# Optimization experiments

Measured on AMD Instinct MI355X. Metric: run time of the kernel, lower is better.

## Reference

```python
import jax, jax.numpy as jnp
import numpy as np

N_NODES = 50000
N_EDGES = 800000
D_IN = 128
H = 4
F = 16


def setup_inputs() -> dict:
    key = jax.random.key(0)
    k1, k2, k3, k4 = jax.random.split(key, 4)
    feat = jax.random.normal(k1, (N_NODES, D_IN), dtype=jnp.float32)
    W = jax.random.normal(k2, (D_IN, H * F), dtype=jnp.float32) / np.sqrt(D_IN)
    src = jax.random.randint(k3, (N_EDGES,), 0, N_NODES, dtype=jnp.int32)
    dst = jax.random.randint(k4, (N_EDGES,), 0, N_NODES, dtype=jnp.int32)
    return {"feat": feat, "W": W, "src": src, "dst": dst}


def reference(feat, W, src, dst):
    # Project: [N, D_in] @ [D_in, H*F] -> [N, H, F]
    ft = (feat @ W).reshape(N_NODES, H, F)
    # Per-edge dot-product scores, scaled: [E, H]
    e = jnp.einsum('ehf,ehf->eh', ft[src], ft[dst]) / np.sqrt(F).astype(np.float32)
    # Segment (per-destination) softmax over incoming edges
    seg_max = jax.ops.segment_max(e, dst, num_segments=N_NODES)  # [N, H]
    ex = jnp.exp(e - seg_max[dst])
    denom = jax.ops.segment_sum(ex, dst, num_segments=N_NODES)  # [N, H]
    sa = ex / denom[dst]  # [E, H]
    # Weighted scatter-sum of source features: [N, H, F]
    msgs = ft[src] * sa[:, :, None]
    out = jax.ops.segment_sum(msgs, dst, num_segments=N_NODES)
    return out
```

## Files before the change

### kernel.cpp

```cpp
#include <hip/hip_runtime.h>
#include <hip/hip_fp16.h>

#define N_NODES 50000
#define N_EDGES 800000
#define D_IN 128
#define HH 4
#define FF 16
#define HF 64
#define NBUCKETS 392
#define BCAP 2560
#define CHUNK 2048
#define NBIN_BLOCKS ((N_EDGES + CHUNK - 1) / CHUNK)
#define GEMM_BLOCKS ((N_NODES + 63) / 64)
#define SORT_K (BCAP / 256)

struct __align__(8) Half4 { __half2 a, b; };

typedef _Float16 half2_v __attribute__((ext_vector_type(2)));
struct __align__(8) H4 { half2_v a, b; };

__device__ __forceinline__ float dot4h(H4 a, H4 v) {
#if __has_builtin(__builtin_amdgcn_fdot2)
    return __builtin_amdgcn_fdot2(a.a, v.a,
           __builtin_amdgcn_fdot2(a.b, v.b, 0.0f, false), false);
#else
    return (float)a.a[0] * (float)v.a[0] + (float)a.a[1] * (float)v.a[1]
         + (float)a.b[0] * (float)v.b[0] + (float)a.b[1] * (float)v.b[1];
#endif
}

__device__ __forceinline__ int block_excl_scan(int val, int* wsum) {
    int lane = threadIdx.x & 63;
    int wave = threadIdx.x >> 6;
    int incl = val;
#pragma unroll
    for (int off = 1; off < 64; off <<= 1) {
        int t = __shfl_up(incl, off, 64);
        if (lane >= off) incl += t;
    }
    if (lane == 63) wsum[wave] = incl;
    __syncthreads();
    if (threadIdx.x == 0) {
        int a = 0;
#pragma unroll
        for (int w = 0; w < 4; ++w) { int t = wsum[w]; wsum[w] = a; a += t; }
    }
    __syncthreads();
    return incl + wsum[wave] - val;
}

union SmemU {
    struct {
        float As[64][132];
        float Bs[D_IN][HF];
    } g;
    struct {
        int hist[512], cur[512], gbase[512];
    } b;
};

__global__ __launch_bounds__(256, 2) void gemm_bin_kernel(const float* __restrict__ feat,
                                                          const float* __restrict__ W,
                                                          const int* __restrict__ src,
                                                          const int* __restrict__ dst,
                                                          __half* __restrict__ fth,
                                                          int* __restrict__ gcur,
                                                          int* __restrict__ recs) {
    __shared__ SmemU smem;
    int tid = threadIdx.x;

    if (blockIdx.x < NBIN_BLOCKS) {
        int e0 = blockIdx.x * CHUNK;
        int n = N_EDGES - e0; if (n > CHUNK) n = CHUNK;

        smem.b.hist[tid] = 0;
        smem.b.hist[tid + 256] = 0;
        __syncthreads();

        int myrec[CHUNK / 256];
        int myb[CHUNK / 256];
#pragma unroll
        for (int k = 0; k < CHUNK / 256; ++k) {
            int idx = tid + k * 256;
            myb[k] = -1;
            if (idx < n) {
                int s = src[e0 + idx];
                int d = dst[e0 + idx];
                int b = d >> 7;
                myrec[k] = s | ((d & 127) << 16) | (b << 23);
                myb[k] = b;
                atomicAdd(&smem.b.hist[b], 1);
            }
        }
        __syncthreads();

#pragma unroll
        for (int j = 0; j < 2; ++j) {
            int idx = tid + j * 256;
            int val = smem.b.hist[idx];
            smem.b.cur[idx] = 0;
            if (val > 0) smem.b.gbase[idx] = atomicAdd(&gcur[idx], val);
        }
        __syncthreads();

#pragma unroll
        for (int k = 0; k < CHUNK / 256; ++k) {
            int b = myb[k];
            if (b >= 0) {
                int pos = smem.b.gbase[b] + atomicAdd(&smem.b.cur[b], 1);
                if (pos < BCAP) recs[(size_t)b * BCAP + pos] = myrec[k];
            }
        }
    } else {
        int gb = blockIdx.x - NBIN_BLOCKS;
        {
            const float4* W4 = (const float4*)W;
            float4* B4 = (float4*)smem.g.Bs;
#pragma unroll
            for (int i = 0; i < 8; ++i) {
                int idx = tid + 256 * i;
                B4[idx] = W4[idx];
            }
        }
        {
            int row0 = gb * 64;
            const float4* F4 = (const float4*)feat;
#pragma unroll
            for (int i = 0; i < 8; ++i) {
                int idx = tid + 256 * i;
                int r = idx >> 5;
                int c4 = idx & 31;
                float4 v = make_float4(0.f, 0.f, 0.f, 0.f);
                int row = row0 + r;
                if (row < N_NODES) v = F4[(size_t)row * 32 + c4];
                *(float4*)&smem.g.As[r][c4 * 4] = v;
            }
        }
        __syncthreads();

        const int tr = tid >> 4;
        const int tc = tid & 15;

        float acc[4][4] = {};
#pragma unroll 8
        for (int k = 0; k < D_IN; k += 4) {
            float av[4][4], bv[4][4];
#pragma unroll
            for (int i = 0; i < 4; ++i) {
                float4 a = *(const float4*)&smem.g.As[tr * 4 + i][k];
                av[i][0] = a.x; av[i][1] = a.y; av[i][2] = a.z; av[i][3] = a.w;
            }
#pragma unroll
            for (int j = 0; j < 4; ++j) {
                float4 b = *(const float4*)&smem.g.Bs[k + j][tc * 4];
                bv[j][0] = b.x; bv[j][1] = b.y; bv[j][2] = b.z; bv[j][3] = b.w;
            }
#pragma unroll
            for (int i = 0; i < 4; ++i)
#pragma unroll
                for (int j = 0; j < 4; ++j)
#pragma unroll
                    for (int c = 0; c < 4; ++c)
                        acc[i][c] = fmaf(av[i][j], bv[j][c], acc[i][c]);
        }

        int row0 = gb * 64;
#pragma unroll
        for (int i = 0; i < 4; ++i) {
            int row = row0 + tr * 4 + i;
            if (row < N_NODES) {
                Half4 h;
                h.a = __floats2half2_rn(acc[i][0], acc[i][1]);
                h.b = __floats2half2_rn(acc[i][2], acc[i][3]);
                *(Half4*)&fth[(size_t)row * HF + tc * 4] = h;
            }
        }
    }
}

__global__ __launch_bounds__(256) void sort_kernel(const int* __restrict__ gcur,
                                                   const int* __restrict__ recs,
                                                   unsigned short* __restrict__ csr,
                                                   int2* __restrict__ rows) {
    __shared__ int lhist[256];
    __shared__ int lcur[256];
    __shared__ int wsum[4];

    int tid = threadIdx.x;
    int b = blockIdx.x;
    int cnt = gcur[b]; if (cnt > BCAP) cnt = BCAP;
    const int* rp = recs + (size_t)b * BCAP;

    lhist[tid] = 0;
    __syncthreads();

    int rk[SORT_K];
#pragma unroll
    for (int k = 0; k < SORT_K; ++k) {
        int i = tid + k * 256;
        bool valid = i < cnt;
        rk[k] = valid ? rp[i] : 0;
        if (valid) atomicAdd(&lhist[(rk[k] >> 16) & 127], 1);
    }
    __syncthreads();

    int val = lhist[tid];
    int excl = block_excl_scan(val, wsum);
    lcur[tid] = excl;
    __syncthreads();

    int base = b * BCAP;
#pragma unroll
    for (int k = 0; k < SORT_K; ++k) {
        int i = tid + k * 256;
        if (i < cnt) {
            int p = atomicAdd(&lcur[(rk[k] >> 16) & 127], 1);
            csr[base + p] = (unsigned short)(rk[k] & 0xFFFF);
        }
    }

    if (tid < 128) {
        int node = (b << 7) + tid;
        if (node < N_NODES) rows[node] = make_int2(base + excl, base + excl + val);
    }
}

__global__ __launch_bounds__(256) void gather_kernel(const __half* __restrict__ fth,
                                                     const int2* __restrict__ rows,
                                                     const unsigned short* __restrict__ csr,
                                                     float* __restrict__ out) {
    int node = __builtin_amdgcn_readfirstlane(blockIdx.x * 4 + (threadIdx.x >> 6));
    int lane = threadIdx.x & 63;
    int g = lane >> 4;
    int hl = lane & 15;

    int2 be = rows[node];
    int beg = be.x;
    int end = be.y;

    H4 a = *(const H4*)&fth[(size_t)node * HF + 4 * hl];

    float acc0 = 0.f, acc1 = 0.f, acc2 = 0.f, acc3 = 0.f, lsum = 0.f;

    for (int i = beg; i < end; i += 16) {
        int s[4];
        bool act[4];
        H4 v[4];
        float p[4];
#pragma unroll
        for (int u = 0; u < 4; ++u) {
            int idx = i + 4 * u + g;
            act[u] = idx < end;
            s[u] = csr[act[u] ? idx : beg];
        }
#pragma unroll
        for (int u = 0; u < 4; ++u) v[u] = *(const H4*)&fth[(size_t)s[u] * HF + 4 * hl];
#pragma unroll
        for (int u = 0; u < 4; ++u) p[u] = dot4h(a, v[u]);
#pragma unroll
        for (int u = 0; u < 4; ++u) p[u] += __shfl_xor(p[u], 1, 64);
#pragma unroll
        for (int u = 0; u < 4; ++u) p[u] += __shfl_xor(p[u], 2, 64);
#pragma unroll
        for (int u = 0; u < 4; ++u) {
            float w = act[u] ? __expf(p[u] * 0.25f) : 0.0f;
            acc0 = fmaf(w, (float)v[u].a[0], acc0);
            acc1 = fmaf(w, (float)v[u].a[1], acc1);
            acc2 = fmaf(w, (float)v[u].b[0], acc2);
            acc3 = fmaf(w, (float)v[u].b[1], acc3);
            lsum += w;
        }
    }

    acc0 += __shfl_xor(acc0, 16, 64);  acc0 += __shfl_xor(acc0, 32, 64);
    acc1 += __shfl_xor(acc1, 16, 64);  acc1 += __shfl_xor(acc1, 32, 64);
    acc2 += __shfl_xor(acc2, 16, 64);  acc2 += __shfl_xor(acc2, 32, 64);
    acc3 += __shfl_xor(acc3, 16, 64);  acc3 += __shfl_xor(acc3, 32, 64);
    lsum += __shfl_xor(lsum, 16, 64);  lsum += __shfl_xor(lsum, 32, 64);

    if (lane < 16) {
        float inv = (lsum > 0.0f) ? 1.0f / lsum : 0.0f;
        *(float4*)&out[(size_t)node * HF + 4 * hl] =
            make_float4(acc0 * inv, acc1 * inv, acc2 * inv, acc3 * inv);
    }
}

extern "C" void kernel_launch(void* const* d_in, const int* in_sizes, int n_in,
                              void* d_out, int out_size, void* d_ws, size_t ws_size,
                              hipStream_t stream) {
    const float* feat = (const float*)d_in[0];
    const float* W = (const float*)d_in[1];
    const int* src = (const int*)d_in[2];
    const int* dst = (const int*)d_in[3];
    float* out = (float*)d_out;

    __half* fth = (__half*)d_ws;
    int* recs = (int*)(fth + (size_t)N_NODES * HF);
    unsigned short* csr = (unsigned short*)(recs + (size_t)NBUCKETS * BCAP);
    int2* rows = (int2*)(csr + (size_t)NBUCKETS * BCAP);
    int* gcur = (int*)(rows + N_NODES);

    hipMemsetAsync(gcur, 0, NBUCKETS * sizeof(int), stream);
    gemm_bin_kernel<<<NBIN_BLOCKS + GEMM_BLOCKS, 256, 0, stream>>>(feat, W, src, dst,
                                                                   fth, gcur, recs);
    sort_kernel<<<NBUCKETS, 256, 0, stream>>>(gcur, recs, csr, rows);
    gather_kernel<<<N_NODES * 64 / 256, 256, 0, stream>>>(fth, rows, csr, out);
}
```

Measured before the change: 138.6 us.

## Split fused GEMM/bin kernel and run projection GEMM in fp16 with fdot2

Splits the combined GEMM-plus-edge-binning launch into two separate kernels launched back-to-back on the same stream. The GEMM now converts feat and W to half in shared memory, stores W transposed, and accumulates with packed fp16 dot2 instructions into fp32. This halves the shared-memory footprint so occupancy can rise to 4 blocks per CU, and it cuts LDS traffic and ALU work. In exchange the two phases no longer overlap inside one grid, there is one extra launch, and rounding the inputs to fp16 before the GEMM lowers precision.

```diff
diff --git a/kernel.cpp b/kernel.cpp
--- a/kernel.cpp
+++ b/kernel.cpp
@@ -19,14 +19,16 @@
 typedef _Float16 half2_v __attribute__((ext_vector_type(2)));
 struct __align__(8) H4 { half2_v a, b; };
 
+__device__ __forceinline__ float dot2acc(half2_v a, half2_v b, float acc) {
+#if __has_builtin(__builtin_amdgcn_fdot2)
+    return __builtin_amdgcn_fdot2(a, b, acc, false);
+#else
+    return acc + (float)a[0] * (float)b[0] + (float)a[1] * (float)b[1];
+#endif
+}
+
 __device__ __forceinline__ float dot4h(H4 a, H4 v) {
-#if __has_builtin(__builtin_amdgcn_fdot2)
-    return __builtin_amdgcn_fdot2(a.a, v.a,
-           __builtin_amdgcn_fdot2(a.b, v.b, 0.0f, false), false);
-#else
-    return (float)a.a[0] * (float)v.a[0] + (float)a.a[1] * (float)v.a[1]
-         + (float)a.b[0] * (float)v.b[0] + (float)a.b[1] * (float)v.b[1];
-#endif
+    return dot2acc(a.a, v.a, dot2acc(a.b, v.b, 0.0f));
 }
 
 __device__ __forceinline__ int block_excl_scan(int val, int* wsum) {
@@ -49,131 +51,124 @@
     return incl + wsum[wave] - val;
 }
 
-union SmemU {
-    struct {
-        float As[64][132];
-        float Bs[D_IN][HF];
-    } g;
-    struct {
-        int hist[512], cur[512], gbase[512];
-    } b;
-};
-
-__global__ __launch_bounds__(256, 2) void gemm_bin_kernel(const float* __restrict__ feat,
-                                                          const float* __restrict__ W,
-                                                          const int* __restrict__ src,
-                                                          const int* __restrict__ dst,
-                                                          __half* __restrict__ fth,
-                                                          int* __restrict__ gcur,
-                                                          int* __restrict__ recs) {
-    __shared__ SmemU smem;
+__global__ __launch_bounds__(256, 4) void gemm_kernel(const float* __restrict__ feat,
+                                                      const float* __restrict__ W,
+                                                      __half* __restrict__ fth) {
+    __shared__ __half As[64][132];
+    __shared__ __half Bst[64][136];
+
     int tid = threadIdx.x;
 
-    if (blockIdx.x < NBIN_BLOCKS) {
-        int e0 = blockIdx.x * CHUNK;
-        int n = N_EDGES - e0; if (n > CHUNK) n = CHUNK;
-
-        smem.b.hist[tid] = 0;
-        smem.b.hist[tid + 256] = 0;
-        __syncthreads();
-
-        int myrec[CHUNK / 256];
-        int myb[CHUNK / 256];
-#pragma unroll
-        for (int k = 0; k < CHUNK / 256; ++k) {
-            int idx = tid + k * 256;
-            myb[k] = -1;
-            if (idx < n) {
-                int s = src[e0 + idx];
-                int d = dst[e0 + idx];
-                int b = d >> 7;
-                myrec[k] = s | ((d & 127) << 16) | (b << 23);
-                myb[k] = b;
-                atomicAdd(&smem.b.hist[b], 1);
-            }
-        }
-        __syncthreads();
-
-#pragma unroll
-        for (int j = 0; j < 2; ++j) {
-            int idx = tid + j * 256;
-            int val = smem.b.hist[idx];
-            smem.b.cur[idx] = 0;
-            if (val > 0) smem.b.gbase[idx] = atomicAdd(&gcur[idx], val);
-        }
-        __syncthreads();
-
-#pragma unroll
-        for (int k = 0; k < CHUNK / 256; ++k) {
-            int b = myb[k];
-            if (b >= 0) {
-                int pos = smem.b.gbase[b] + atomicAdd(&smem.b.cur[b], 1);
-                if (pos < BCAP) recs[(size_t)b * BCAP + pos] = myrec[k];
-            }
-        }
-    } else {
-        int gb = blockIdx.x - NBIN_BLOCKS;
-        {
-            const float4* W4 = (const float4*)W;
-            float4* B4 = (float4*)smem.g.Bs;
-#pragma unroll
-            for (int i = 0; i < 8; ++i) {
-                int idx = tid + 256 * i;
-                B4[idx] = W4[idx];
-            }
-        }
-        {
-            int row0 = gb * 64;
-            const float4* F4 = (const float4*)feat;
-#pragma unroll
-            for (int i = 0; i < 8; ++i) {
-                int idx = tid + 256 * i;
-                int r = idx >> 5;
-                int c4 = idx & 31;
-                float4 v = make_float4(0.f, 0.f, 0.f, 0.f);
-                int row = row0 + r;
-                if (row < N_NODES) v = F4[(size_t)row * 32 + c4];
-                *(float4*)&smem.g.As[r][c4 * 4] = v;
-            }
-        }
-        __syncthreads();
-
-        const int tr = tid >> 4;
-        const int tc = tid & 15;
-
-        float acc[4][4] = {};
-#pragma unroll 8
-        for (int k = 0; k < D_IN; k += 4) {
-            float av[4][4], bv[4][4];
-#pragma unroll
-            for (int i = 0; i < 4; ++i) {
-                float4 a = *(const float4*)&smem.g.As[tr * 4 + i][k];
-                av[i][0] = a.x; av[i][1] = a.y; av[i][2] = a.z; av[i][3] = a.w;
-            }
-#pragma unroll
-            for (int j = 0; j < 4; ++j) {
-                float4 b = *(const float4*)&smem.g.Bs[k + j][tc * 4];
-                bv[j][0] = b.x; bv[j][1] = b.y; bv[j][2] = b.z; bv[j][3] = b.w;
-            }
-#pragma unroll
-            for (int i = 0; i < 4; ++i)
-#pragma unroll
-                for (int j = 0; j < 4; ++j)
-#pragma unroll
-                    for (int c = 0; c < 4; ++c)
-                        acc[i][c] = fmaf(av[i][j], bv[j][c], acc[i][c]);
-        }
-
-        int row0 = gb * 64;
-#pragma unroll
-        for (int i = 0; i < 4; ++i) {
-            int row = row0 + tr * 4 + i;
-            if (row < N_NODES) {
-                Half4 h;
-                h.a = __floats2half2_rn(acc[i][0], acc[i][1]);
-                h.b = __floats2half2_rn(acc[i][2], acc[i][3]);
-                *(Half4*)&fth[(size_t)row * HF + tc * 4] = h;
-            }
+    {
+        const float4* W4 = (const float4*)W;
+#pragma unroll
+        for (int i = 0; i < 8; ++i) {
+            int idx = tid + 256 * i;
+            int k = idx >> 4;
+            int c4 = idx & 15;
+            float4 v = W4[idx];
+            Bst[c4 * 4 + 0][k] = __float2half(v.x);
+            Bst[c4 * 4 + 1][k] = __float2half(v.y);
+            Bst[c4 * 4 + 2][k] = __float2half(v.z);
+            Bst[c4 * 4 + 3][k] = __float2half(v.w);
+        }
+    }
+    {
+        int row0 = blockIdx.x * 64;
+        const float4* F4 = (const float4*)feat;
+#pragma unroll
+        for (int i = 0; i < 8; ++i) {
+            int idx = tid + 256 * i;
+            int r = idx >> 5;
+            int c4 = idx & 31;
+            float4 v = make_float4(0.f, 0.f, 0.f, 0.f);
+            int row = row0 + r;
+            if (row < N_NODES) v = F4[(size_t)row * 32 + c4];
+            Half4 h;
+            h.a = __floats2half2_rn(v.x, v.y);
+            h.b = __floats2half2_rn(v.z, v.w);
+            *(Half4*)&As[r][c4 * 4] = h;
+        }
+    }
+    __syncthreads();
+
+    const int tr = tid >> 4;
+    const int tc = tid & 15;
+
+    float acc[4][4] = {};
+#pragma unroll 4
+    for (int k4 = 0; k4 < D_IN / 4; ++k4) {
+        H4 a[4], b[4];
+#pragma unroll
+        for (int i = 0; i < 4; ++i) a[i] = *(const H4*)&As[tr * 4 + i][k4 * 4];
+#pragma unroll
+        for (int c = 0; c < 4; ++c) b[c] = *(const H4*)&Bst[tc * 4 + c][k4 * 4];
+#pragma unroll
+        for (int i = 0; i < 4; ++i)
+#pragma unroll
+            for (int c = 0; c < 4; ++c)
+                acc[i][c] = dot2acc(a[i].b, b[c].b, dot2acc(a[i].a, b[c].a, acc[i][c]));
+    }
+
+    int row0 = blockIdx.x * 64;
+#pragma unroll
+    for (int i = 0; i < 4; ++i) {
+        int row = row0 + tr * 4 + i;
+        if (row < N_NODES) {
+            Half4 h;
+            h.a = __floats2half2_rn(acc[i][0], acc[i][1]);
+            h.b = __floats2half2_rn(acc[i][2], acc[i][3]);
+            *(Half4*)&fth[(size_t)row * HF + tc * 4] = h;
+        }
+    }
+}
+
+__global__ __launch_bounds__(256) void bin_kernel(const int* __restrict__ src,
+                                                  const int* __restrict__ dst,
+                                                  int* __restrict__ gcur,
+                                                  int* __restrict__ recs) {
+    __shared__ int hist[512], cur[512], gbase[512];
+
+    int tid = threadIdx.x;
+    int e0 = blockIdx.x * CHUNK;
+    int n = N_EDGES - e0; if (n > CHUNK) n = CHUNK;
+
+    hist[tid] = 0;
+    hist[tid + 256] = 0;
+    __syncthreads();
+
+    int myrec[CHUNK / 256];
+    int myb[CHUNK / 256];
+#pragma unroll
+    for (int k = 0; k < CHUNK / 256; ++k) {
+        int idx = tid + k * 256;
+        myb[k] = -1;
+        if (idx < n) {
+            int s = src[e0 + idx];
+            int d = dst[e0 + idx];
+            int b = d >> 7;
+            myrec[k] = s | ((d & 127) << 16) | (b << 23);
+            myb[k] = b;
+            atomicAdd(&hist[b], 1);
+        }
+    }
+    __syncthreads();
+
+#pragma unroll
+    for (int j = 0; j < 2; ++j) {
+        int idx = tid + j * 256;
+        int val = hist[idx];
+        cur[idx] = 0;
+        if (val > 0) gbase[idx] = atomicAdd(&gcur[idx], val);
+    }
+    __syncthreads();
+
+#pragma unroll
+    for (int k = 0; k < CHUNK / 256; ++k) {
+        int b = myb[k];
+        if (b >= 0) {
+            int pos = gbase[b] + atomicAdd(&cur[b], 1);
+            if (pos < BCAP) recs[(size_t)b * BCAP + pos] = myrec[k];
         }
     }
 }
@@ -301,8 +296,8 @@
     int* gcur = (int*)(rows + N_NODES);
 
     hipMemsetAsync(gcur, 0, NBUCKETS * sizeof(int), stream);
-    gemm_bin_kernel<<<NBIN_BLOCKS + GEMM_BLOCKS, 256, 0, stream>>>(feat, W, src, dst,
-                                                                   fth, gcur, recs);
+    gemm_kernel<<<GEMM_BLOCKS, 256, 0, stream>>>(feat, W, fth);
+    bin_kernel<<<NBIN_BLOCKS, 256, 0, stream>>>(src, dst, gcur, recs);
     sort_kernel<<<NBUCKETS, 256, 0, stream>>>(gcur, recs, csr, rows);
     gather_kernel<<<N_NODES * 64 / 256, 256, 0, stream>>>(fth, rows, csr, out);
 }
```

Result: no change. 138.0 us (-0.4%).

## Stage GEMM operands as fp16 in shared memory and use packed dot2

Applied to the files above, without the earlier changes.

The projection GEMM now converts feat and W to half precision when staging them into shared memory, with W stored transposed so each thread reads contiguous k-slices. The inner loop uses fdot2 packed half dot products with fp32 accumulation instead of scalar fp32 FMAs. This halves LDS footprint and instruction count, and the launch bound is raised to 4 blocks per SM to increase occupancy. It rounds inputs to fp16 before the multiply, which slightly reduces accuracy. The transposed W store is a strided scalar write pattern that may cause bank conflicts.

```diff
diff --git a/kernel.cpp b/kernel.cpp
--- a/kernel.cpp
+++ b/kernel.cpp
@@ -19,14 +19,16 @@
 typedef _Float16 half2_v __attribute__((ext_vector_type(2)));
 struct __align__(8) H4 { half2_v a, b; };
 
+__device__ __forceinline__ float dot2acc(half2_v a, half2_v b, float acc) {
+#if __has_builtin(__builtin_amdgcn_fdot2)
+    return __builtin_amdgcn_fdot2(a, b, acc, false);
+#else
+    return acc + (float)a[0] * (float)b[0] + (float)a[1] * (float)b[1];
+#endif
+}
+
 __device__ __forceinline__ float dot4h(H4 a, H4 v) {
-#if __has_builtin(__builtin_amdgcn_fdot2)
-    return __builtin_amdgcn_fdot2(a.a, v.a,
-           __builtin_amdgcn_fdot2(a.b, v.b, 0.0f, false), false);
-#else
-    return (float)a.a[0] * (float)v.a[0] + (float)a.a[1] * (float)v.a[1]
-         + (float)a.b[0] * (float)v.b[0] + (float)a.b[1] * (float)v.b[1];
-#endif
+    return dot2acc(a.a, v.a, dot2acc(a.b, v.b, 0.0f));
 }
 
 __device__ __forceinline__ int block_excl_scan(int val, int* wsum) {
@@ -51,15 +53,15 @@
 
 union SmemU {
     struct {
-        float As[64][132];
-        float Bs[D_IN][HF];
+        __half As[64][132];
+        __half Bst[64][136];
     } g;
     struct {
         int hist[512], cur[512], gbase[512];
     } b;
 };
 
-__global__ __launch_bounds__(256, 2) void gemm_bin_kernel(const float* __restrict__ feat,
+__global__ __launch_bounds__(256, 4) void gemm_bin_kernel(const float* __restrict__ feat,
                                                           const float* __restrict__ W,
                                                           const int* __restrict__ src,
                                                           const int* __restrict__ dst,
@@ -113,13 +115,19 @@
         }
     } else {
         int gb = blockIdx.x - NBIN_BLOCKS;
+
         {
             const float4* W4 = (const float4*)W;
-            float4* B4 = (float4*)smem.g.Bs;
 #pragma unroll
             for (int i = 0; i < 8; ++i) {
                 int idx = tid + 256 * i;
-                B4[idx] = W4[idx];
+                int k = idx >> 4;
+                int c4 = idx & 15;
+                float4 v = W4[idx];
+                smem.g.Bst[c4 * 4 + 0][k] = __float2half(v.x);
+                smem.g.Bst[c4 * 4 + 1][k] = __float2half(v.y);
+                smem.g.Bst[c4 * 4 + 2][k] = __float2half(v.z);
+                smem.g.Bst[c4 * 4 + 3][k] = __float2half(v.w);
             }
         }
         {
@@ -133,7 +141,10 @@
                 float4 v = make_float4(0.f, 0.f, 0.f, 0.f);
                 int row = row0 + r;
                 if (row < N_NODES) v = F4[(size_t)row * 32 + c4];
-                *(float4*)&smem.g.As[r][c4 * 4] = v;
+                Half4 h;
+                h.a = __floats2half2_rn(v.x, v.y);
+                h.b = __floats2half2_rn(v.z, v.w);
+                *(Half4*)&smem.g.As[r][c4 * 4] = h;
             }
         }
         __syncthreads();
@@ -142,26 +153,18 @@
         const int tc = tid & 15;
 
         float acc[4][4] = {};
-#pragma unroll 8
-        for (int k = 0; k < D_IN; k += 4) {
-            float av[4][4], bv[4][4];
-#pragma unroll
-            for (int i = 0; i < 4; ++i) {
-                float4 a = *(const float4*)&smem.g.As[tr * 4 + i][k];
-                av[i][0] = a.x; av[i][1] = a.y; av[i][2] = a.z; av[i][3] = a.w;
-            }
-#pragma unroll
-            for (int j = 0; j < 4; ++j) {
-                float4 b = *(const float4*)&smem.g.Bs[k + j][tc * 4];
-                bv[j][0] = b.x; bv[j][1] = b.y; bv[j][2] = b.z; bv[j][3] = b.w;
-            }
+#pragma unroll 4
+        for (int k4 = 0; k4 < D_IN / 4; ++k4) {
+            H4 a[4], b[4];
+#pragma unroll
+            for (int i = 0; i < 4; ++i) a[i] = *(const H4*)&smem.g.As[tr * 4 + i][k4 * 4];
+#pragma unroll
+            for (int c = 0; c < 4; ++c) b[c] = *(const H4*)&smem.g.Bst[tc * 4 + c][k4 * 4];
 #pragma unroll
             for (int i = 0; i < 4; ++i)
 #pragma unroll
-                for (int j = 0; j < 4; ++j)
-#pragma unroll
-                    for (int c = 0; c < 4; ++c)
-                        acc[i][c] = fmaf(av[i][j], bv[j][c], acc[i][c]);
+                for (int c = 0; c < 4; ++c)
+                    acc[i][c] = dot2acc(a[i].b, b[c].b, dot2acc(a[i].a, b[c].a, acc[i][c]));
         }
 
         int row0 = gb * 64;
```

Result: slower. 152.5 us (+10.0%).
